# Performance work log

Measured on AMD Instinct MI355X. Metric: run time of the kernel, lower is better.

The kernel has to match this reference:

```python
import jax, jax.numpy as jnp
import numpy as np

IN_FEATURES = 512
OUT_FEATURES = 256
BATCH = 1024


def setup_inputs() -> dict:
    key = jax.random.key(0)
    k1, k2, k3, k4 = jax.random.split(key, 4)
    n_lower = IN_FEATURES * (IN_FEATURES - 1) // 2  # strictly-lower triangle count
    return {
        "inputs": jax.random.normal(k1, (BATCH, IN_FEATURES), dtype=jnp.float32),
        "weight": jax.random.normal(k2, (OUT_FEATURES, 1, IN_FEATURES), dtype=jnp.float32),
        "L_diags": jax.random.uniform(k3, (OUT_FEATURES, IN_FEATURES), dtype=jnp.float32),
        "L_lower": jax.random.normal(k4, (OUT_FEATURES, n_lower), dtype=jnp.float32) * 0.05,
    }


def _build_L(L_diags, L_lower):
    # Per-class lower-triangular matrix: diag = L_diags**2, strict lower = L_lower.
    K, d = L_diags.shape
    ri, ci = np.tril_indices(d, k=-1)  # static index pattern (row-major, matches torch.tril_indices)
    diag_idx = jnp.arange(d)
    L = jnp.zeros((K, d, d), dtype=L_diags.dtype)
    L = L.at[:, diag_idx, diag_idx].set(jnp.square(L_diags))
    L = L.at[:, ri, ci].set(L_lower)
    return L  # [K, d, d]


def reference(inputs, weight, L_diags, L_lower):
    L = _build_L(L_diags, L_lower)                      # [K, d, d]
    pinputs = jnp.einsum('bd,kde->kbe', inputs, L)      # [K, B, d]
    pweights = jnp.einsum('kod,kde->koe', weight, L)    # [K, 1, d]
    dist = pinputs - pweights                           # broadcast over B -> [K, B, d]
    out = jnp.sqrt(jnp.sum(jnp.square(dist), axis=2))   # torch.norm(dim=2) -> [K, B]
    return out.T                                        # [B, K]
```

## Files before the change

### kernel.cpp

```cpp
#include <hip/hip_runtime.h>
#include <hip/hip_bf16.h>
#include <math.h>

#define B_SZ   1024
#define D_SZ   512
#define KC_SZ  256
#define NLOW   130816

#define STEP_ELEMS  8192
#define NSTEPS      20
#define CLASS_ELEMS (NSTEPS * STEP_ELEMS)

#define OFF_XP     (size_t)(KC_SZ * CLASS_ELEMS * 2)
#define OFF_TPART  (OFF_XP + 64 * STEP_ELEMS * 2)
#define OFF_T      (OFF_TPART + (size_t)KC_SZ * 8 * 512 * 4)
#define WS_NEED    (OFF_T + (size_t)KC_SZ * 512 * 4)

typedef __attribute__((ext_vector_type(4))) float  f32x4;
typedef __attribute__((ext_vector_type(4), aligned(4))) float f32x4u;
typedef __attribute__((ext_vector_type(8))) __bf16 bf16x8;

__device__ __forceinline__ int sbase_of(int ct) { return ct * (9 - ct); }
__device__ __forceinline__ int kch_of(int s) {
    return (s < 8) ? s : (s < 14) ? s - 6 : (s < 18) ? s - 10 : s - 12;
}

__global__ __launch_bounds__(256)
void prep_x(const float* __restrict__ X, __hip_bfloat16* __restrict__ Xp) {
    const int bx  = blockIdx.x;
    const int pg  = bx >> 2;
    const int mt  = pg >> 3, kch = pg & 7;
    __bf16* out = (__bf16*)Xp + (size_t)pg * STEP_ELEMS;
    const int line = threadIdx.x + (bx & 3) * 256;
    const int wmg = line >> 9, mi = (line >> 7) & 3, h = (line >> 6) & 1;
    const int lane = line & 63, q = lane >> 4, c = lane & 15;
    const int row = mt * 128 + wmg * 64 + mi * 16 + c;
    const float* src = X + (size_t)row * D_SZ + kch * 64 + h * 32 + q * 8;
    f32x4 v0 = ((const f32x4*)src)[0];
    f32x4 v1 = ((const f32x4*)src)[1];
    bf16x8 p;
    #pragma unroll
    for (int j = 0; j < 4; ++j) { p[j] = (__bf16)v0[j]; p[j + 4] = (__bf16)v1[j]; }
    *(bf16x8*)(out + line * 8) = p;
}

__global__ __launch_bounds__(256)
void prep_b(const float* __restrict__ Ldiag,
            const float* __restrict__ Llow,
            const float* __restrict__ W,
            __hip_bfloat16* __restrict__ Bp,
            float* __restrict__ tpart) {
    __shared__ __bf16 Lt[128 * 64];
    __shared__ float  ptl[32 * 129];

    const int s  = blockIdx.x;
    const int kc = blockIdx.y;
    const int ct = (s < 8) ? 0 : (s < 14) ? 1 : (s < 18) ? 2 : 3;
    const int dt = kch_of(s);
    const int e0 = ct << 7, d0 = dt << 6;

    const int tid = threadIdx.x;
    const int m   = tid & 31;
    const int seg = tid >> 5;
    const int es  = seg << 4;
    const int dg0 = d0 + 2 * m;

    int cls;
    if (dt >= 2 * ct + 2)      cls = 0;
    else if (dt == 2 * ct + 1) cls = (seg < 4) ? 0 : 1;
    else                       cls = (seg < 4) ? 1 : 2;

    const float* lowb = Llow + (size_t)kc * NLOW;
    const float2 wv = *(const float2*)(W + (size_t)kc * D_SZ + dg0);

    float v0[16], v1[16];
    if (cls == 0) {
        const int t0 = (dg0 * (dg0 - 1)) >> 1;
        const int t1 = t0 + dg0;
        const float* s0 = lowb + t0 + e0 + es;
        const float* s1 = lowb + t1 + e0 + es;
        #pragma unroll
        for (int i = 0; i < 4; ++i) {
            f32x4u a = ((const f32x4u*)s0)[i];
            f32x4u b = ((const f32x4u*)s1)[i];
            #pragma unroll
            for (int j = 0; j < 4; ++j) { v0[i * 4 + j] = a[j]; v1[i * 4 + j] = b[j]; }
        }
    } else if (cls == 1) {
        const int t0 = (dg0 * (dg0 - 1)) >> 1;
        const int t1 = t0 + dg0;
        const float* diagb = Ldiag + (size_t)kc * D_SZ;
        float q0 = diagb[dg0],     q1 = diagb[dg0 + 1];
        q0 *= q0; q1 *= q1;
        #pragma unroll
        for (int j = 0; j < 16; ++j) {
            const int eg = e0 + es + j;
            v0[j] = (eg < dg0)     ? lowb[t0 + eg] : ((eg == dg0)     ? q0 : 0.f);
            v1[j] = (eg < dg0 + 1) ? lowb[t1 + eg] : ((eg == dg0 + 1) ? q1 : 0.f);
        }
    } else {
        #pragma unroll
        for (int j = 0; j < 16; ++j) { v0[j] = 0.f; v1[j] = 0.f; }
    }

    char* ltb = (char*)Lt;
    #pragma unroll
    for (int j = 0; j < 16; ++j) {
        const int el = es + j;
        union { __bf16 h[2]; unsigned u; } pk;
        pk.h[0] = (__bf16)v0[j];
        pk.h[1] = (__bf16)v1[j];
        const int off = el * 128 + ((4 * m) ^ ((el & 7) << 4));
        *(unsigned*)(ltb + off) = pk.u;
        ptl[m * 129 + el] = wv.x * v0[j] + wv.y * v1[j];
    }
    __syncthreads();

    __bf16* page = (__bf16*)Bp + (size_t)kc * CLASS_ELEMS + (size_t)s * STEP_ELEMS;
    const int lane = tid & 63, q = lane >> 4, c = lane & 15;
    #pragma unroll
    for (int k = 0; k < 4; ++k) {
        const int ln = k * 256 + tid;
        const int up = ln >> 6;
        const int h  = up & 1;
        const int el = ((up >> 3) << 6) + (((up >> 1) & 3) << 4) + c;
        const int off = el * 128 + (((h << 6) + (q << 4)) ^ ((el & 7) << 4));
        *(bf16x8*)(page + (size_t)ln * 8) = *(const bf16x8*)(ltb + off);
    }

    if (tid < 128) {
        float sum = 0.f;
        #pragma unroll
        for (int mm = 0; mm < 32; ++mm) sum += ptl[mm * 129 + tid];
        tpart[((size_t)(kc * 8 + dt)) * 512 + e0 + tid] = sum;
    }
}

__global__ __launch_bounds__(256)
void t_reduce(const float* __restrict__ tpart, float* __restrict__ Tv) {
    const int idx = blockIdx.x * 256 + threadIdx.x;
    const int kc = idx >> 9, e = idx & 511;
    const int ct = e >> 7;
    float s = 0.f;
    for (int dt = ct << 1; dt < 8; ++dt)
        s += tpart[((size_t)(kc * 8 + dt)) * 512 + e];
    Tv[idx] = s;
}

__global__ __launch_bounds__(256, 2)
void gml2_main(const __hip_bfloat16* __restrict__ Xp,
               const __hip_bfloat16* __restrict__ Bp,
               const float* __restrict__ Tv,
               float* __restrict__ Out) {
    __shared__ float osum[2][128];

    const int tid = threadIdx.x;
    const int bx  = blockIdx.x;
    const int xcd = bx & 7;
    const int g   = bx >> 3;
    const int kc  = xcd * 32 + (g >> 3);
    const int mt  = g & 7;

    const int lane = tid & 63;
    const int wave = tid >> 6;
    const int wmg  = wave & 1;
    const int wng  = wave >> 1;
    const int c    = lane & 15;
    const int q    = lane >> 4;

    const __bf16* pA = (const __bf16*)Xp + (size_t)(mt * 8) * STEP_ELEMS;
    const __bf16* pB = (const __bf16*)Bp + (size_t)kc * CLASS_ELEMS;

    int aoff[4][2], boff[4][2];
    #pragma unroll
    for (int mi = 0; mi < 4; ++mi)
        #pragma unroll
        for (int h = 0; h < 2; ++h)
            aoff[mi][h] = ((((wmg * 4 + mi) * 2 + h) * 64) + lane) * 8;
    #pragma unroll
    for (int ni = 0; ni < 4; ++ni)
        #pragma unroll
        for (int h = 0; h < 2; ++h)
            boff[ni][h] = ((((wng * 4 + ni) * 2 + h) * 64) + lane) * 8;

    f32x4 acc[4][4];
    #pragma unroll
    for (int mi = 0; mi < 4; ++mi)
        #pragma unroll
        for (int ni = 0; ni < 4; ++ni)
            acc[mi][ni] = (f32x4){0.f, 0.f, 0.f, 0.f};
    float rsum[16];
    #pragma unroll
    for (int i = 0; i < 16; ++i) rsum[i] = 0.f;

    bf16x8 fa0[4][2], fb0[4][2], fa1[4][2], fb1[4][2];

#define LOAD_A(FA, KCH) { const __bf16* p_ = pA + (KCH) * STEP_ELEMS;          \
    _Pragma("unroll") for (int mi = 0; mi < 4; ++mi)                           \
    _Pragma("unroll") for (int h = 0; h < 2; ++h)                              \
        FA[mi][h] = *(const bf16x8*)(p_ + aoff[mi][h]); }
#define LOAD_B(FB, SP) { const __bf16* p_ = pB + (SP) * STEP_ELEMS;            \
    _Pragma("unroll") for (int ni = 0; ni < 4; ++ni)                           \
    _Pragma("unroll") for (int h = 0; h < 2; ++h)                              \
        FB[ni][h] = *(const bf16x8*)(p_ + boff[ni][h]); }
#define MFMA_STEP(FA, FB)                                                      \
    _Pragma("unroll") for (int mi = 0; mi < 4; ++mi)                           \
    _Pragma("unroll") for (int ni = 0; ni < 4; ++ni)                           \
    _Pragma("unroll") for (int h = 0; h < 2; ++h)                              \
        acc[mi][ni] = __builtin_amdgcn_mfma_f32_16x16x32_bf16(                 \
            FA[mi][h], FB[ni][h], acc[mi][ni], 0, 0, 0);

#define FOLD(CT) {                                                             \
    float tv_[4];                                                              \
    _Pragma("unroll") for (int ni = 0; ni < 4; ++ni)                           \
        tv_[ni] = Tv[kc * 512 + (CT) * 128 + wng * 64 + ni * 16 + c];          \
    _Pragma("unroll") for (int mi = 0; mi < 4; ++mi)                           \
    _Pragma("unroll") for (int ni = 0; ni < 4; ++ni)                           \
    _Pragma("unroll") for (int r = 0; r < 4; ++r) {                            \
        float y_ = acc[mi][ni][r] - tv_[ni];                                   \
        rsum[mi * 4 + r] += y_ * y_;                                           \
        acc[mi][ni][r] = 0.f; } }

    LOAD_A(fa0, 0); LOAD_B(fb0, 0);

    for (int s = 0; s < NSTEPS; s += 2) {
        if (s == 8)       { FOLD(0); }
        else if (s == 14) { FOLD(1); }
        else if (s == 18) { FOLD(2); }

        LOAD_A(fa1, kch_of(s + 1)); LOAD_B(fb1, s + 1);
        MFMA_STEP(fa0, fb0);
        if (s + 2 < NSTEPS) { LOAD_A(fa0, kch_of(s + 2)); LOAD_B(fb0, s + 2); }
        MFMA_STEP(fa1, fb1);
    }
    FOLD(3);

    #pragma unroll
    for (int i = 0; i < 16; ++i) {
        float v = rsum[i];
        v += __shfl_xor(v, 1, 64);
        v += __shfl_xor(v, 2, 64);
        v += __shfl_xor(v, 4, 64);
        v += __shfl_xor(v, 8, 64);
        rsum[i] = v;
    }
    if (c == 0) {
        #pragma unroll
        for (int mi = 0; mi < 4; ++mi)
            #pragma unroll
            for (int r = 0; r < 4; ++r)
                osum[wng][wmg * 64 + mi * 16 + q * 4 + r] = rsum[mi * 4 + r];
    }
    __syncthreads();
    if (tid < 128) {
        float v = osum[0][tid] + osum[1][tid];
        Out[(size_t)(mt * 128 + tid) * KC_SZ + kc] = sqrtf(v);
    }
}

#define FLDA 40
#define BM 128
#define BN 128
__device__ __forceinline__ void fstep_map(int s, int& ct, int& k0) {
    if (s < 16)      { ct = 0; k0 = s * 32; }
    else if (s < 28) { ct = 1; k0 = 128 + (s - 16) * 32; }
    else if (s < 36) { ct = 2; k0 = 256 + (s - 28) * 32; }
    else             { ct = 3; k0 = 384 + (s - 36) * 32; }
}
__global__ __launch_bounds__(256, 2)
void gml2_fallback(const float* __restrict__ X, const float* __restrict__ W,
                   const float* __restrict__ Ldiag, const float* __restrict__ Llow,
                   float* __restrict__ Out) {
    __shared__ __bf16 As[BM * FLDA];
    __shared__ __bf16 Bs[BN * FLDA];
    __shared__ float  Ws[D_SZ];
    __shared__ float  osum[2][BM];
    const int tid = threadIdx.x;
    const int bx  = blockIdx.x;
    const int xcd = bx & 7;
    const int g   = bx >> 3;
    const int kc  = xcd * 32 + (g >> 3);
    const int mt  = g & 7;
    const int lane = tid & 63, wave = tid >> 6;
    const int wm = (wave & 1) * 64, wn = (wave >> 1) * 64;
    const int c = lane & 15, q = lane >> 4;
    const int am = tid >> 1, akh = (tid & 1) << 4;
    const float* xrow = X + (size_t)(mt * BM + am) * D_SZ;
    const float* wrow = W + (size_t)kc * D_SZ;
    const int be = tid & 127, bd = (tid >> 7) << 4;
    const float* lowbase  = Llow  + (size_t)kc * NLOW;
    const float* diagbase = Ldiag + (size_t)kc * D_SZ;
    if (tid < 128) ((f32x4*)Ws)[tid] = ((const f32x4*)wrow)[tid];
    float rsum[16];
    #pragma unroll
    for (int i = 0; i < 16; ++i) rsum[i] = 0.f;
    f32x4 acc[4][4];
    #pragma unroll
    for (int mi = 0; mi < 4; ++mi)
        #pragma unroll
        for (int ni = 0; ni < 4; ++ni) acc[mi][ni] = (f32x4){0.f, 0.f, 0.f, 0.f};
    f32x4 xr[4];
    float bb[16];
    auto prefetch = [&](int s) {
        int pct, pk0; fstep_map(s, pct, pk0);
        const int pe0 = pct * BN;
        const float* xp = xrow + pk0 + akh;
        #pragma unroll
        for (int i = 0; i < 4; ++i) xr[i] = ((const f32x4*)xp)[i];
        const int e = pe0 + be, d0 = pk0 + bd;
        int tri = (d0 * (d0 - 1)) >> 1;
        if (pk0 >= pe0 + BN) {
            #pragma unroll
            for (int j = 0; j < 16; ++j) { bb[j] = lowbase[tri + e]; tri += d0 + j; }
        } else {
            #pragma unroll
            for (int j = 0; j < 16; ++j) {
                const int d = d0 + j;
                float val = 0.f;
                if (d > e)       val = lowbase[tri + e];
                else if (d == e) { float dq = diagbase[d]; val = dq * dq; }
                bb[j] = val; tri += d;
            }
        }
    };
    prefetch(0);
    __syncthreads();
    int cur_ct = 0;
    for (int s = 0; s < 40; ++s) {
        int ct, k0; fstep_map(s, ct, k0);
        if (ct != cur_ct) {
            #pragma unroll
            for (int mi = 0; mi < 4; ++mi)
                #pragma unroll
                for (int ni = 0; ni < 4; ++ni)
                    #pragma unroll
                    for (int r = 0; r < 4; ++r) {
                        float y = acc[mi][ni][r];
                        rsum[mi * 4 + r] += y * y;
                        acc[mi][ni][r] = 0.f;
                    }
            cur_ct = ct;
        }
        bf16x8 ap0, ap1;
        {
            const f32x4* wsp = (const f32x4*)&Ws[k0 + akh];
            #pragma unroll
            for (int i = 0; i < 4; ++i) {
                f32x4 wv = wsp[i];
                #pragma unroll
                for (int l = 0; l < 4; ++l) {
                    float v = xr[i][l] - wv[l];
                    int idx = i * 4 + l;
                    if (idx < 8) ap0[idx] = (__bf16)v;
                    else         ap1[idx - 8] = (__bf16)v;
                }
            }
        }
        bf16x8 bp0, bp1;
        #pragma unroll
        for (int j = 0; j < 8; ++j) { bp0[j] = (__bf16)bb[j]; bp1[j] = (__bf16)bb[j + 8]; }
        __syncthreads();
        *(bf16x8*)&As[am * FLDA + akh]     = ap0;
        *(bf16x8*)&As[am * FLDA + akh + 8] = ap1;
        *(bf16x8*)&Bs[be * FLDA + bd]      = bp0;
        *(bf16x8*)&Bs[be * FLDA + bd + 8]  = bp1;
        if (s + 1 < 40) prefetch(s + 1);
        __syncthreads();
        bf16x8 af[4], bfr[4];
        #pragma unroll
        for (int mi = 0; mi < 4; ++mi)
            af[mi] = *(const bf16x8*)&As[(wm + mi * 16 + c) * FLDA + q * 8];
        #pragma unroll
        for (int ni = 0; ni < 4; ++ni)
            bfr[ni] = *(const bf16x8*)&Bs[(wn + ni * 16 + c) * FLDA + q * 8];
        #pragma unroll
        for (int mi = 0; mi < 4; ++mi)
            #pragma unroll
            for (int ni = 0; ni < 4; ++ni)
                acc[mi][ni] = __builtin_amdgcn_mfma_f32_16x16x32_bf16(
                    af[mi], bfr[ni], acc[mi][ni], 0, 0, 0);
    }
    #pragma unroll
    for (int mi = 0; mi < 4; ++mi)
        #pragma unroll
        for (int ni = 0; ni < 4; ++ni)
            #pragma unroll
            for (int r = 0; r < 4; ++r) {
                float y = acc[mi][ni][r];
                rsum[mi * 4 + r] += y * y;
            }
    #pragma unroll
    for (int i = 0; i < 16; ++i) {
        float s = rsum[i];
        s += __shfl_xor(s, 1, 64);
        s += __shfl_xor(s, 2, 64);
        s += __shfl_xor(s, 4, 64);
        s += __shfl_xor(s, 8, 64);
        rsum[i] = s;
    }
    const int wnIdx = wave >> 1;
    if (c == 0) {
        #pragma unroll
        for (int mi = 0; mi < 4; ++mi)
            #pragma unroll
            for (int r = 0; r < 4; ++r)
                osum[wnIdx][wm + mi * 16 + q * 4 + r] = rsum[mi * 4 + r];
    }
    __syncthreads();
    if (tid < BM) {
        float s = osum[0][tid] + osum[1][tid];
        Out[(size_t)(mt * BM + tid) * KC_SZ + kc] = sqrtf(s);
    }
}

extern "C" void kernel_launch(void* const* d_in, const int* in_sizes, int n_in,
                              void* d_out, int out_size, void* d_ws, size_t ws_size,
                              hipStream_t stream) {
    const float* X  = (const float*)d_in[0];
    const float* W  = (const float*)d_in[1];
    const float* Ld = (const float*)d_in[2];
    const float* Ll = (const float*)d_in[3];
    float* Out = (float*)d_out;

    if (ws_size >= WS_NEED) {
        __hip_bfloat16* Bp    = (__hip_bfloat16*)d_ws;
        __hip_bfloat16* Xp    = (__hip_bfloat16*)((char*)d_ws + OFF_XP);
        float*          tpart = (float*)((char*)d_ws + OFF_TPART);
        float*          Tvv   = (float*)((char*)d_ws + OFF_T);
        prep_x  <<<dim3(256),           dim3(256), 0, stream>>>(X, Xp);
        prep_b  <<<dim3(NSTEPS, KC_SZ), dim3(256), 0, stream>>>(Ld, Ll, W, Bp, tpart);
        t_reduce<<<dim3(512),           dim3(256), 0, stream>>>(tpart, Tvv);
        gml2_main<<<dim3(KC_SZ * 8),    dim3(256), 0, stream>>>(Xp, Bp, Tvv, Out);
    } else {
        gml2_fallback<<<dim3(KC_SZ * 8), dim3(256), 0, stream>>>(X, W, Ld, Ll, Out);
    }
}
```

Measured before the change: 327.4 us.

## Keep all A fragments in registers and stage B tiles through LDS asynchronously

Preloads all eight A-operand k-chunks into registers once and reuses them across the triangular step schedule, so A is no longer reloaded from global memory each step. The per-class B tiles are now double-buffered in shared memory using global_load_lds, with explicit vmcnt waits and barriers around each step. The T vector is also cached in LDS. This greatly raises register pressure (64 bf16x8 fragments per thread) and adds two barriers per step, which risks spills or lower occupancy at launch_bounds(256,2).

```diff
diff --git a/kernel.cpp b/kernel.cpp
--- a/kernel.cpp
+++ b/kernel.cpp
@@ -152,6 +152,8 @@
                const __hip_bfloat16* __restrict__ Bp,
                const float* __restrict__ Tv,
                float* __restrict__ Out) {
+    __shared__ __align__(16) char bbuf[2][16384];
+    __shared__ float tvs[512];
     __shared__ float osum[2][128];
 
     const int tid = threadIdx.x;
@@ -171,17 +173,18 @@
     const __bf16* pA = (const __bf16*)Xp + (size_t)(mt * 8) * STEP_ELEMS;
     const __bf16* pB = (const __bf16*)Bp + (size_t)kc * CLASS_ELEMS;
 
-    int aoff[4][2], boff[4][2];
-    #pragma unroll
-    for (int mi = 0; mi < 4; ++mi)
-        #pragma unroll
-        for (int h = 0; h < 2; ++h)
-            aoff[mi][h] = ((((wmg * 4 + mi) * 2 + h) * 64) + lane) * 8;
-    #pragma unroll
-    for (int ni = 0; ni < 4; ++ni)
-        #pragma unroll
-        for (int h = 0; h < 2; ++h)
-            boff[ni][h] = ((((wng * 4 + ni) * 2 + h) * 64) + lane) * 8;
+    if (tid < 128) ((f32x4*)tvs)[tid] = ((const f32x4*)(Tv + kc * 512))[tid];
+
+    bf16x8 fa0[4][2], fa1[4][2], fa2[4][2], fa3[4][2],
+           fa5[4][2], fa4[4][2], fa6[4][2], fa7[4][2];
+#define LOAD_FA(NAME, KCH) {                                                   \
+    const __bf16* p_ = pA + (size_t)(KCH) * STEP_ELEMS;                        \
+    _Pragma("unroll") for (int mi = 0; mi < 4; ++mi)                           \
+    _Pragma("unroll") for (int h = 0; h < 2; ++h)                              \
+        NAME[mi][h] = *(const bf16x8*)(p_ +                                    \
+            ((((wmg * 4 + mi) * 2 + h) * 64) + lane) * 8); }
+    LOAD_FA(fa0, 0) LOAD_FA(fa1, 1) LOAD_FA(fa2, 2) LOAD_FA(fa3, 3)
+    LOAD_FA(fa4, 4) LOAD_FA(fa5, 5) LOAD_FA(fa6, 6) LOAD_FA(fa7, 7)
 
     f32x4 acc[4][4];
     #pragma unroll
@@ -193,27 +196,40 @@
     #pragma unroll
     for (int i = 0; i < 16; ++i) rsum[i] = 0.f;
 
-    bf16x8 fa0[4][2], fb0[4][2], fa1[4][2], fb1[4][2];
-
-#define LOAD_A(FA, KCH) { const __bf16* p_ = pA + (KCH) * STEP_ELEMS;          \
-    _Pragma("unroll") for (int mi = 0; mi < 4; ++mi)                           \
-    _Pragma("unroll") for (int h = 0; h < 2; ++h)                              \
-        FA[mi][h] = *(const bf16x8*)(p_ + aoff[mi][h]); }
-#define LOAD_B(FB, SP) { const __bf16* p_ = pB + (SP) * STEP_ELEMS;            \
+#define STAGE_B(BUF, SP) {                                                     \
+    const char* gb_ = (const char*)(pB + (size_t)(SP) * STEP_ELEMS);           \
+    char* lb_ = &bbuf[BUF][0];                                                 \
+    _Pragma("unroll") for (int i_ = 0; i_ < 4; ++i_) {                         \
+        const int ch_ = (wave * 4 + i_) * 1024;                                \
+        __builtin_amdgcn_global_load_lds(                                      \
+            (const __attribute__((address_space(1))) void*)(gb_ + ch_ + lane * 16), \
+            (__attribute__((address_space(3))) void*)(lb_ + ch_), 16, 0, 0);   \
+    } }
+
+#define GSTEP(S, FA) {                                                         \
+    if ((S) + 1 < NSTEPS) {                                                    \
+        STAGE_B(((S) & 1) ^ 1, (S) + 1);                                       \
+        asm volatile("s_waitcnt vmcnt(4)" ::: "memory");                       \
+    } else {                                                                   \
+        asm volatile("s_waitcnt vmcnt(0)" ::: "memory");                       \
+    }                                                                          \
+    __builtin_amdgcn_s_barrier();                                              \
+    bf16x8 fb[4][2];                                                           \
     _Pragma("unroll") for (int ni = 0; ni < 4; ++ni)                           \
     _Pragma("unroll") for (int h = 0; h < 2; ++h)                              \
-        FB[ni][h] = *(const bf16x8*)(p_ + boff[ni][h]); }
-#define MFMA_STEP(FA, FB)                                                      \
+        fb[ni][h] = *(const bf16x8*)(&bbuf[(S) & 1][0] +                       \
+            ((((wng * 4 + ni) * 2 + h) * 64) + lane) * 16);                    \
+    _Pragma("unroll") for (int h = 0; h < 2; ++h)                              \
     _Pragma("unroll") for (int mi = 0; mi < 4; ++mi)                           \
     _Pragma("unroll") for (int ni = 0; ni < 4; ++ni)                           \
-    _Pragma("unroll") for (int h = 0; h < 2; ++h)                              \
         acc[mi][ni] = __builtin_amdgcn_mfma_f32_16x16x32_bf16(                 \
-            FA[mi][h], FB[ni][h], acc[mi][ni], 0, 0, 0);
+            FA[mi][h], fb[ni][h], acc[mi][ni], 0, 0, 0);                       \
+    __builtin_amdgcn_s_barrier(); }
 
 #define FOLD(CT) {                                                             \
     float tv_[4];                                                              \
     _Pragma("unroll") for (int ni = 0; ni < 4; ++ni)                           \
-        tv_[ni] = Tv[kc * 512 + (CT) * 128 + wng * 64 + ni * 16 + c];          \
+        tv_[ni] = tvs[(CT) * 128 + wng * 64 + ni * 16 + c];                    \
     _Pragma("unroll") for (int mi = 0; mi < 4; ++mi)                           \
     _Pragma("unroll") for (int ni = 0; ni < 4; ++ni)                           \
     _Pragma("unroll") for (int r = 0; r < 4; ++r) {                            \
@@ -221,19 +237,18 @@
         rsum[mi * 4 + r] += y_ * y_;                                           \
         acc[mi][ni][r] = 0.f; } }
 
-    LOAD_A(fa0, 0); LOAD_B(fb0, 0);
-
-    for (int s = 0; s < NSTEPS; s += 2) {
-        if (s == 8)       { FOLD(0); }
-        else if (s == 14) { FOLD(1); }
-        else if (s == 18) { FOLD(2); }
-
-        LOAD_A(fa1, kch_of(s + 1)); LOAD_B(fb1, s + 1);
-        MFMA_STEP(fa0, fb0);
-        if (s + 2 < NSTEPS) { LOAD_A(fa0, kch_of(s + 2)); LOAD_B(fb0, s + 2); }
-        MFMA_STEP(fa1, fb1);
-    }
-    FOLD(3);
+    STAGE_B(0, 0);
+
+    GSTEP(0,  fa0) GSTEP(1,  fa1) GSTEP(2,  fa2) GSTEP(3,  fa3)
+    GSTEP(4,  fa4) GSTEP(5,  fa5) GSTEP(6,  fa6) GSTEP(7,  fa7)
+    FOLD(0)
+    GSTEP(8,  fa2) GSTEP(9,  fa3) GSTEP(10, fa4) GSTEP(11, fa5)
+    GSTEP(12, fa6) GSTEP(13, fa7)
+    FOLD(1)
+    GSTEP(14, fa4) GSTEP(15, fa5) GSTEP(16, fa6) GSTEP(17, fa7)
+    FOLD(2)
+    GSTEP(18, fa6) GSTEP(19, fa7)
+    FOLD(3)
 
     #pragma unroll
     for (int i = 0; i < 16; ++i) {
```

After: 469.0 us. 43.3% more time.
